# Kernel tuning notes

Measured on AMD Instinct MI355X. Metric: run time of the kernel, lower is better.

## Reference

```python
import jax, jax.numpy as jnp
import numpy as np

LAYER_SIZE = 8
STACK_SIZE = 2
RES_CH = 64
SKIP_CH = 128
N = 16
L = 8192
NUM_BLOCKS = LAYER_SIZE * STACK_SIZE


def _dilations():
    return [2 ** lev for _ in range(STACK_SIZE) for lev in range(LAYER_SIZE)]


def setup_inputs() -> dict:
    key = jax.random.key(0)
    k1, k2, k3, k4 = jax.random.split(key, 4)
    x = jax.random.normal(k1, (N, RES_CH, L), dtype=jnp.float32)
    # conv weights scaled ~1/sqrt(fan_in) to keep gates in a sane range
    W_dil = jax.random.normal(k2, (NUM_BLOCKS, RES_CH, RES_CH, 2), dtype=jnp.float32) * 0.088
    W_res = jax.random.normal(k3, (NUM_BLOCKS, RES_CH, RES_CH), dtype=jnp.float32) * 0.125
    W_skip = jax.random.normal(k4, (NUM_BLOCKS, SKIP_CH, RES_CH), dtype=jnp.float32) * 0.125
    return {"x": x, "W_dil": W_dil, "W_res": W_res, "W_skip": W_skip}


def reference(x, W_dil, W_res, W_skip):
    dilations = _dilations()
    out = x
    skips = []
    for i, d in enumerate(dilations):
        wd = W_dil[i]    # (Cout, Cin, 2)
        wr = W_res[i]    # (C, C) 1x1
        ws = W_skip[i]   # (S, C) 1x1
        # dilated causal conv, kernel_size=2, no padding -> length L-d
        y = (jnp.einsum('oi,nil->nol', wd[:, :, 0], out[:, :, :-d])
             + jnp.einsum('oi,nil->nol', wd[:, :, 1], out[:, :, d:]))
        # gated activation: tanh and sigmoid of the SAME dilated output
        g = jnp.tanh(y) * jax.nn.sigmoid(y)
        # NOTE: source has `if self.pooling > 1` with self.pooling a bool,
        # so AvgPool1d is never applied; pool_out == g always.
        res = jnp.einsum('oi,nil->nol', wr, g) + out[:, :, -g.shape[2]:]
        skips.append(jnp.einsum('oi,nil->nol', ws, g))
        out = res
    osize = out.shape[2]
    skip_out = skips[0][:, :, -osize:]
    for s in skips[1:]:
        skip_out = skip_out + s[:, :, -osize:]
    return (out, skip_out)
```

## Files before the change

### kernel.cpp

```cpp
#include <hip/hip_runtime.h>
#include <hip/hip_cooperative_groups.h>

namespace cg = cooperative_groups;


#define NBATCH 16
#define C 64
#define SC 128
#define L0 8192
#define OSIZE 7682
#define TILE 64
#define ST 128
#define FT 256
#define FW 384
#define FSMEM (8*FW*8*2 + 8*FT*8*2)

typedef __bf16 bf16x8 __attribute__((ext_vector_type(8)));
typedef __bf16 bf16x4 __attribute__((ext_vector_type(4)));
typedef float  f32x4  __attribute__((ext_vector_type(4)));

__global__ __launch_bounds__(256) void pack_weights(
    const float* __restrict__ Wd, const float* __restrict__ Wr,
    const float* __restrict__ Ws,
    __bf16* __restrict__ Wdm, __bf16* __restrict__ Wrm, __bf16* __restrict__ Wsm)
{
    int idx = blockIdx.x * 256 + threadIdx.x;
    if (idx < 131072) {
        int kp = idx & 127, o = (idx >> 7) & 63, ly = idx >> 13;
        int k = kp & 63, tap = kp >> 6;
        Wdm[idx] = (__bf16)Wd[(((ly * 64 + o) * 64 + k) << 1) + tap];
    } else if (idx < 196608) {
        int j = idx - 131072;
        Wrm[j] = (__bf16)Wr[j];
    } else if (idx < 327680) {
        int j = idx - 196608;
        Wsm[j] = (__bf16)Ws[j];
    }
}

__global__ __launch_bounds__(256, 2) void wavenet_fused(
    const float* __restrict__ x,
    float* __restrict__ bufA, float* __restrict__ bufB,
    const __bf16* __restrict__ Wdm, const __bf16* __restrict__ Wrm,
    const __bf16* __restrict__ Wsm,
    float* __restrict__ out, float* __restrict__ skip)
{
    extern __shared__ char smem[];
    __bf16* sxp = (__bf16*)smem;
    __bf16* sgp = (__bf16*)(smem + 8 * FW * 8 * 2);

    cg::grid_group gg = cg::this_grid();

    const int blk = blockIdx.x;
    const int n   = blk >> 5;
    const int a   = (blk & 31) * FT;
    const int t    = threadIdx.x;
    const int lane = t & 63;
    const int wv   = t >> 6;
    const int q    = lane >> 4;
    const int nn   = lane & 15;

    f32x4 accS[2][16];
    #pragma unroll
    for (int mt = 0; mt < 2; ++mt)
        #pragma unroll
        for (int nt = 0; nt < 16; ++nt)
            accS[mt][nt] = (f32x4){0.f, 0.f, 0.f, 0.f};

    const float* src = x;

    for (int ly = 0; ly < 16; ++ly) {
        const int d = 1 << (ly & 7);
        const int W = FT + d;

        for (int kg = 0; kg < 8; ++kg) {
            for (int j = t; j < W; j += 256) {
                int s = a - d + j;
                if (s < 0) s = 0;
                const float* col = src + (size_t)(n * C + kg * 8) * L0 + s;
                bf16x8 bv;
                #pragma unroll
                for (int jj = 0; jj < 8; ++jj) bv[jj] = (__bf16)col[(size_t)jj * L0];
                *(bf16x8*)(sxp + ((size_t)kg * FW + j) * 8) = bv;
            }
        }
        __syncthreads();

        const __bf16* arow = Wdm + ((size_t)ly * 64 + (wv * 16 + nn)) * 128 + q * 8;
        bf16x8 aW0 = *(const bf16x8*)(arow);
        bf16x8 aW1 = *(const bf16x8*)(arow + 32);
        bf16x8 aW2 = *(const bf16x8*)(arow + 64);
        bf16x8 aW3 = *(const bf16x8*)(arow + 96);
        #pragma unroll 4
        for (int nt = 0; nt < 16; ++nt) {
            int p = nt * 16 + nn;
            f32x4 acc = {0.f, 0.f, 0.f, 0.f};
            acc = __builtin_amdgcn_mfma_f32_16x16x32_bf16(aW0,
                    *(const bf16x8*)(sxp + ((size_t)(q    ) * FW + p    ) * 8), acc, 0, 0, 0);
            acc = __builtin_amdgcn_mfma_f32_16x16x32_bf16(aW1,
                    *(const bf16x8*)(sxp + ((size_t)(4 + q) * FW + p    ) * 8), acc, 0, 0, 0);
            acc = __builtin_amdgcn_mfma_f32_16x16x32_bf16(aW2,
                    *(const bf16x8*)(sxp + ((size_t)(q    ) * FW + p + d) * 8), acc, 0, 0, 0);
            acc = __builtin_amdgcn_mfma_f32_16x16x32_bf16(aW3,
                    *(const bf16x8*)(sxp + ((size_t)(4 + q) * FW + p + d) * 8), acc, 0, 0, 0);
            bf16x4 gv;
            #pragma unroll
            for (int r = 0; r < 4; ++r) {
                float y = fminf(fmaxf(acc[r], -20.f), 20.f);
                float u = __expf(y);
                gv[r] = (__bf16)(u * (u - 1.f) / fmaf(u, u, 1.f));
            }
            *(bf16x4*)(sgp + ((size_t)(2 * wv + (q >> 1)) * FT + p) * 8 + (q & 1) * 4) = gv;
        }
        __syncthreads();

        const __bf16* rrow = Wrm + ((size_t)ly * 64 + (wv * 16 + nn)) * 64 + q * 8;
        bf16x8 aR0 = *(const bf16x8*)rrow;
        bf16x8 aR1 = *(const bf16x8*)(rrow + 32);
        float* dst = (ly & 1) ? bufB : bufA;
        #pragma unroll 4
        for (int nt = 0; nt < 16; ++nt) {
            int p = nt * 16 + nn;
            f32x4 acc = {0.f, 0.f, 0.f, 0.f};
            acc = __builtin_amdgcn_mfma_f32_16x16x32_bf16(aR0,
                    *(const bf16x8*)(sgp + ((size_t)(q    ) * FT + p) * 8), acc, 0, 0, 0);
            acc = __builtin_amdgcn_mfma_f32_16x16x32_bf16(aR1,
                    *(const bf16x8*)(sgp + ((size_t)(4 + q) * FT + p) * 8), acc, 0, 0, 0);
            int s = a + p;
            if (ly == 15) {
                if (s >= 510) {
                    #pragma unroll
                    for (int r = 0; r < 4; ++r) {
                        int ch = wv * 16 + q * 4 + r;
                        out[(size_t)(n * C + ch) * OSIZE + (s - 510)]
                            = acc[r] + src[(size_t)(n * C + ch) * L0 + s];
                    }
                }
            } else {
                #pragma unroll
                for (int r = 0; r < 4; ++r) {
                    int ch = wv * 16 + q * 4 + r;
                    dst[(size_t)(n * C + ch) * L0 + s]
                        = acc[r] + src[(size_t)(n * C + ch) * L0 + s];
                }
            }
        }

        const __bf16* srow = Wsm + (size_t)ly * SC * 64;
        bf16x8 aS00 = *(const bf16x8*)(srow + (size_t)(wv * 32 +      nn) * 64 +      q * 8);
        bf16x8 aS01 = *(const bf16x8*)(srow + (size_t)(wv * 32 +      nn) * 64 + 32 + q * 8);
        bf16x8 aS10 = *(const bf16x8*)(srow + (size_t)(wv * 32 + 16 + nn) * 64 +      q * 8);
        bf16x8 aS11 = *(const bf16x8*)(srow + (size_t)(wv * 32 + 16 + nn) * 64 + 32 + q * 8);
        #pragma unroll
        for (int nt = 0; nt < 16; ++nt) {
            int p = nt * 16 + nn;
            bf16x8 b0 = *(const bf16x8*)(sgp + ((size_t)(q    ) * FT + p) * 8);
            bf16x8 b1 = *(const bf16x8*)(sgp + ((size_t)(4 + q) * FT + p) * 8);
            accS[0][nt] = __builtin_amdgcn_mfma_f32_16x16x32_bf16(aS00, b0, accS[0][nt], 0, 0, 0);
            accS[0][nt] = __builtin_amdgcn_mfma_f32_16x16x32_bf16(aS01, b1, accS[0][nt], 0, 0, 0);
            accS[1][nt] = __builtin_amdgcn_mfma_f32_16x16x32_bf16(aS10, b0, accS[1][nt], 0, 0, 0);
            accS[1][nt] = __builtin_amdgcn_mfma_f32_16x16x32_bf16(aS11, b1, accS[1][nt], 0, 0, 0);
        }

        src = dst;
        if (ly < 15) gg.sync();
    }

    #pragma unroll
    for (int mt = 0; mt < 2; ++mt)
        #pragma unroll
        for (int nt = 0; nt < 16; ++nt) {
            int s = a + nt * 16 + nn;
            if (s >= 510) {
                #pragma unroll
                for (int r = 0; r < 4; ++r) {
                    int sch = wv * 32 + mt * 16 + q * 4 + r;
                    skip[(size_t)(n * SC + sch) * OSIZE + (s - 510)] = accS[mt][nt][r];
                }
            }
        }
}

__global__ __launch_bounds__(256) void wavenet_layer_mfma(
    const float* __restrict__ src, int src_stride, int Lin,
    float* __restrict__ dst, int dst_stride,
    const __bf16* __restrict__ Wdm,
    const __bf16* __restrict__ Wrm,
    __bf16* __restrict__ gout,
    int d)
{
    extern __shared__ char smem_raw[];
    const int W    = TILE + d;
    const int Lout = Lin - d;
    const int n  = blockIdx.y;
    const int l0 = blockIdx.x * TILE;
    if (l0 >= Lout) return;
    const int np = min(TILE, Lout - l0);

    __bf16* sxp  = (__bf16*)smem_raw;
    float*  sres = (float*)(smem_raw + (size_t)8 * W * 8 * 2);
    __bf16* sgp  = (__bf16*)(sres + 64 * 65);

    const int t    = threadIdx.x;
    const int lane = t & 63;
    const int wv   = t >> 6;
    const int q    = lane >> 4;
    const int nn   = lane & 15;

    for (int item = t; item < 8 * W; item += 256) {
        int kg = item / W;
        int p  = item % W;
        bool inb = (l0 + p) < Lin;
        const float* col = src + (size_t)(n * C + kg * 8) * src_stride + l0 + p;
        float v[8];
        #pragma unroll
        for (int j = 0; j < 8; ++j) v[j] = inb ? col[(size_t)j * src_stride] : 0.f;
        bf16x8 bv;
        #pragma unroll
        for (int j = 0; j < 8; ++j) bv[j] = (__bf16)v[j];
        *(bf16x8*)(sxp + ((size_t)kg * W + p) * 8) = bv;
        int pr = p - d;
        if (pr >= 0 && pr < TILE) {
            #pragma unroll
            for (int j = 0; j < 8; ++j) sres[(kg * 8 + j) * 65 + pr] = v[j];
        }
    }
    __syncthreads();

    const __bf16* arow = Wdm + (size_t)(wv * 16 + nn) * 128 + q * 8;
    bf16x8 aW[4];
    #pragma unroll
    for (int ks = 0; ks < 4; ++ks) aW[ks] = *(const bf16x8*)(arow + ks * 32);

    #pragma unroll
    for (int nt = 0; nt < 4; ++nt) {
        int p0 = nt * 16;
        f32x4 acc = {0.f, 0.f, 0.f, 0.f};
        acc = __builtin_amdgcn_mfma_f32_16x16x32_bf16(aW[0],
                *(const bf16x8*)(sxp + ((size_t)(q    ) * W + p0 + nn    ) * 8), acc, 0, 0, 0);
        acc = __builtin_amdgcn_mfma_f32_16x16x32_bf16(aW[1],
                *(const bf16x8*)(sxp + ((size_t)(4 + q) * W + p0 + nn    ) * 8), acc, 0, 0, 0);
        acc = __builtin_amdgcn_mfma_f32_16x16x32_bf16(aW[2],
                *(const bf16x8*)(sxp + ((size_t)(q    ) * W + p0 + nn + d) * 8), acc, 0, 0, 0);
        acc = __builtin_amdgcn_mfma_f32_16x16x32_bf16(aW[3],
                *(const bf16x8*)(sxp + ((size_t)(4 + q) * W + p0 + nn + d) * 8), acc, 0, 0, 0);
        bf16x4 gv;
        #pragma unroll
        for (int r = 0; r < 4; ++r) {
            float y = fminf(fmaxf(acc[r], -20.f), 20.f);
            float u = __expf(y);
            gv[r] = (__bf16)(u * (u - 1.f) / fmaf(u, u, 1.f));
        }
        *(bf16x4*)(sgp + ((size_t)(2 * wv + (q >> 1)) * 64 + p0 + nn) * 8 + (q & 1) * 4) = gv;
    }
    __syncthreads();

    const __bf16* rrow = Wrm + (size_t)(wv * 16 + nn) * 64 + q * 8;
    bf16x8 aR0 = *(const bf16x8*)rrow;
    bf16x8 aR1 = *(const bf16x8*)(rrow + 32);
    #pragma unroll
    for (int nt = 0; nt < 4; ++nt) {
        int p0 = nt * 16;
        f32x4 acc = {0.f, 0.f, 0.f, 0.f};
        acc = __builtin_amdgcn_mfma_f32_16x16x32_bf16(aR0,
                *(const bf16x8*)(sgp + ((size_t)(q    ) * 64 + p0 + nn) * 8), acc, 0, 0, 0);
        acc = __builtin_amdgcn_mfma_f32_16x16x32_bf16(aR1,
                *(const bf16x8*)(sgp + ((size_t)(4 + q) * 64 + p0 + nn) * 8), acc, 0, 0, 0);
        if (p0 + nn < np) {
            #pragma unroll
            for (int r = 0; r < 4; ++r) {
                int ch = wv * 16 + q * 4 + r;
                dst[(size_t)(n * C + ch) * dst_stride + l0 + p0 + nn]
                    = acc[r] + sres[ch * 65 + p0 + nn];
            }
        }
    }

    const int sbase = Lout - OSIZE;
    for (int item = t; item < 8 * TILE; item += 256) {
        int p  = item & 63;
        int kg = item >> 6;
        int l  = l0 + p;
        if (l >= sbase && l < Lout) {
            *(bf16x8*)(gout + (((size_t)n * 8 + kg) * OSIZE + (l - sbase)) * 8)
                = *(const bf16x8*)(sgp + ((size_t)kg * 64 + p) * 8);
        }
    }
}

__global__ __launch_bounds__(256) void skip_gemm(
    const __bf16* __restrict__ g,
    const __bf16* __restrict__ Wsm,
    float* __restrict__ skip,
    int G, int lybase, int init)
{
    __shared__ __bf16 Bb[8][ST][8];
    const int n  = blockIdx.y;
    const int l0 = blockIdx.x * ST;
    const int t  = threadIdx.x;
    const int lane = t & 63;
    const int wv   = __builtin_amdgcn_readfirstlane(t >> 6);
    const int q = lane >> 4, nn = lane & 15;

    f32x4 acc[2][8];
    #pragma unroll
    for (int mt = 0; mt < 2; ++mt)
        #pragma unroll
        for (int nt = 0; nt < 8; ++nt) acc[mt][nt] = (f32x4){0.f, 0.f, 0.f, 0.f};

    for (int gi = 0; gi < G; ++gi) {
        const __bf16* gl = g + ((size_t)gi * NBATCH + n) * (size_t)8 * OSIZE * 8;
        #pragma unroll
        for (int j = 0; j < 4; ++j) {
            int kg   = 2 * wv + (j >> 1);
            int half = j & 1;
            const __bf16* srcp = gl + ((size_t)kg * OSIZE + l0 + half * 64) * 8
                                    + (size_t)lane * 8;
            __builtin_amdgcn_global_load_lds(
                (const __attribute__((address_space(1))) void*)srcp,
                (__attribute__((address_space(3))) void*)&Bb[kg][half * 64][0],
                16, 0, 0);
        }
        const __bf16* Wl = Wsm + (size_t)(lybase + gi) * SC * 64;
        bf16x8 a00 = *(const bf16x8*)(Wl + (size_t)(wv * 32 +      nn) * 64 +  0 + q * 8);
        bf16x8 a01 = *(const bf16x8*)(Wl + (size_t)(wv * 32 +      nn) * 64 + 32 + q * 8);
        bf16x8 a10 = *(const bf16x8*)(Wl + (size_t)(wv * 32 + 16 + nn) * 64 +  0 + q * 8);
        bf16x8 a11 = *(const bf16x8*)(Wl + (size_t)(wv * 32 + 16 + nn) * 64 + 32 + q * 8);
        __syncthreads();
        #pragma unroll
        for (int ks = 0; ks < 2; ++ks) {
            #pragma unroll
            for (int nt = 0; nt < 8; ++nt) {
                bf16x8 b = *(const bf16x8*)&Bb[ks * 4 + q][nt * 16 + nn][0];
                acc[0][nt] = __builtin_amdgcn_mfma_f32_16x16x32_bf16(
                                 ks ? a01 : a00, b, acc[0][nt], 0, 0, 0);
                acc[1][nt] = __builtin_amdgcn_mfma_f32_16x16x32_bf16(
                                 ks ? a11 : a10, b, acc[1][nt], 0, 0, 0);
            }
        }
        __syncthreads();
    }

    #pragma unroll
    for (int mt = 0; mt < 2; ++mt)
        #pragma unroll
        for (int nt = 0; nt < 8; ++nt) {
            int p = l0 + nt * 16 + nn;
            if (p < OSIZE) {
                #pragma unroll
                for (int r = 0; r < 4; ++r) {
                    int s = wv * 32 + mt * 16 + q * 4 + r;
                    size_t idx = ((size_t)n * SC + s) * OSIZE + p;
                    float v = acc[mt][nt][r];
                    skip[idx] = init ? v : (skip[idx] + v);
                }
            }
        }
}

extern "C" void kernel_launch(void* const* d_in, const int* in_sizes, int n_in,
                              void* d_out, int out_size, void* d_ws, size_t ws_size,
                              hipStream_t stream) {
    const float* x      = (const float*)d_in[0];
    const float* W_dil  = (const float*)d_in[1];
    const float* W_res  = (const float*)d_in[2];
    const float* W_skip = (const float*)d_in[3];

    float* out  = (float*)d_out;
    float* skip = out + (size_t)NBATCH * C * OSIZE;

    float*  bufA = (float*)d_ws;
    float*  bufB = bufA + (size_t)NBATCH * C * L0;
    __bf16* Wdm  = (__bf16*)(bufB + (size_t)NBATCH * C * L0);
    __bf16* Wrm  = Wdm + 16 * 64 * 128;
    __bf16* Wsm  = Wrm + 16 * 64 * 64;
    __bf16* gst  = Wsm + 16 * 128 * 64;

    static int use_coop = -1;
    if (use_coop < 0) {
        int dev = 0, coop = 0, nb = 0;
        hipGetDevice(&dev);
        hipDeviceGetAttribute(&coop, hipDeviceAttributeCooperativeLaunch, dev);
        hipError_t e = hipOccupancyMaxActiveBlocksPerMultiprocessor(
            &nb, (const void*)wavenet_fused, 256, FSMEM);
        use_coop = (coop && e == hipSuccess && nb >= 2) ? 1 : 0;
    }

    pack_weights<<<1280, 256, 0, stream>>>(W_dil, W_res, W_skip, Wdm, Wrm, Wsm);

    if (use_coop) {
        void* args[] = { (void*)&x, (void*)&bufA, (void*)&bufB,
                         (void*)&Wdm, (void*)&Wrm, (void*)&Wsm,
                         (void*)&out, (void*)&skip };
        hipLaunchCooperativeKernel((const void*)wavenet_fused,
                                   dim3(NBATCH * (L0 / FT)), dim3(256),
                                   args, FSMEM, stream);
        return;
    }

    const size_t slotHW = (size_t)NBATCH * 8 * OSIZE * 8;
    const size_t used   = (size_t)((char*)gst - (char*)d_ws);
    int G = 16;
    while (G > 1 && used + (size_t)G * slotHW * 2 + 65536 > ws_size) G >>= 1;

    const float* src = x;
    int src_stride = L0, Lin = L0;
    float* bufs[2] = {bufA, bufB};

    for (int i = 0; i < 16; ++i) {
        int d    = 1 << (i & 7);
        int Lout = Lin - d;
        float* dst;
        int dst_stride;
        if (i == 15) { dst = out;         dst_stride = OSIZE; }
        else         { dst = bufs[i & 1]; dst_stride = L0;    }

        int W = TILE + d;
        size_t smem = (size_t)128 * W + 64 * 65 * 4 + 8 * 64 * 8 * 2;

        dim3 grid((Lout + TILE - 1) / TILE, NBATCH);
        wavenet_layer_mfma<<<grid, 256, smem, stream>>>(
            src, src_stride, Lin, dst, dst_stride,
            Wdm + (size_t)i * 64 * 128,
            Wrm + (size_t)i * 64 * 64,
            gst + (size_t)(i % G) * slotHW,
            d);

        if (((i + 1) % G) == 0) {
            dim3 sgrid((OSIZE + ST - 1) / ST, NBATCH);
            skip_gemm<<<sgrid, 256, 0, stream>>>(
                gst, Wsm, skip, G, i + 1 - G, (i + 1 == G) ? 1 : 0);
        }

        src = dst;
        src_stride = dst_stride;
        Lin = Lout;
    }
}
```

Measured before the change: 601.3 us.

## Keep residual in registers and batch small-dilation layers with halo recompute

Each block now holds its residual tile in fp32 registers across layers instead of round-tripping through global buffers every layer. Layers with dilation 1–16 are run back-to-back on a 32-column halo staged once, recomputing the halo residuals locally in shared memory. This removes most grid-wide syncs and global writes and reads. Grid syncs and boundary writes to global memory remain only for the large-dilation layers. The cost is extra halo compute, more register pressure (xs plus accS), and larger shared memory use.

```diff
diff --git a/kernel.cpp b/kernel.cpp
--- a/kernel.cpp
+++ b/kernel.cpp
@@ -12,8 +12,7 @@
 #define TILE 64
 #define ST 128
 #define FT 256
-#define FW 384
-#define FSMEM (8*FW*8*2 + 8*FT*8*2)
+#define FSMEM 81920
 
 typedef __bf16 bf16x8 __attribute__((ext_vector_type(8)));
 typedef __bf16 bf16x4 __attribute__((ext_vector_type(4)));
@@ -40,69 +39,93 @@
 
 __global__ __launch_bounds__(256, 2) void wavenet_fused(
     const float* __restrict__ x,
-    float* __restrict__ bufA, float* __restrict__ bufB,
+    float* __restrict__ bufH0, float* __restrict__ bufH1,
     const __bf16* __restrict__ Wdm, const __bf16* __restrict__ Wrm,
     const __bf16* __restrict__ Wsm,
     float* __restrict__ out, float* __restrict__ skip)
 {
     extern __shared__ char smem[];
-    __bf16* sxp = (__bf16*)smem;
-    __bf16* sgp = (__bf16*)(smem + 8 * FW * 8 * 2);
-
     cg::grid_group gg = cg::this_grid();
 
-    const int blk = blockIdx.x;
-    const int n   = blk >> 5;
-    const int a   = (blk & 31) * FT;
+    const int blk  = blockIdx.x;
+    const int n    = blk >> 5;
+    const int a    = (blk & 31) * FT;
     const int t    = threadIdx.x;
     const int lane = t & 63;
     const int wv   = t >> 6;
     const int q    = lane >> 4;
     const int nn   = lane & 15;
-
+    const int kgw  = 2 * wv + (q >> 1);
+    const int hf4  = (q & 1) * 4;
+
+    f32x4 xs[16];
     f32x4 accS[2][16];
     #pragma unroll
     for (int mt = 0; mt < 2; ++mt)
         #pragma unroll
-        for (int nt = 0; nt < 16; ++nt)
-            accS[mt][nt] = (f32x4){0.f, 0.f, 0.f, 0.f};
-
-    const float* src = x;
-
-    for (int ly = 0; ly < 16; ++ly) {
-        const int d = 1 << (ly & 7);
-        const int W = FT + d;
-
-        for (int kg = 0; kg < 8; ++kg) {
-            for (int j = t; j < W; j += 256) {
-                int s = a - d + j;
-                if (s < 0) s = 0;
-                const float* col = src + (size_t)(n * C + kg * 8) * L0 + s;
-                bf16x8 bv;
+        for (int vt = 0; vt < 16; ++vt) accS[mt][vt] = (f32x4){0.f, 0.f, 0.f, 0.f};
+
+    #pragma unroll
+    for (int vt = 0; vt < 16; ++vt) {
+        const float* p = x + (size_t)(n * C + wv * 16 + q * 4) * L0 + a + vt * 16 + nn;
+        #pragma unroll
+        for (int r = 0; r < 4; ++r) xs[vt][r] = p[(size_t)r * L0];
+    }
+
+    __bf16* sxp = (__bf16*)smem;
+
+    auto stage_valid = [&](int SW, int SXO) {
+        #pragma unroll
+        for (int vt = 0; vt < 16; ++vt) {
+            bf16x4 v;
+            #pragma unroll
+            for (int r = 0; r < 4; ++r) v[r] = (__bf16)xs[vt][r];
+            *(bf16x4*)(sxp + (kgw * SW + SXO + vt * 16 + nn) * 8 + hf4) = v;
+        }
+    };
+    auto stage_halo = [&](int SW, int PH, const float* src, int H, int lg) {
+        for (int it = t; it < 8 * H; it += 256) {
+            int kg = it >> lg, hj = it & (H - 1);
+            int s = a - H + hj; if (s < 0) s = 0;
+            const float* col = src + (size_t)(n * C + kg * 8) * L0 + s;
+            bf16x8 bv;
+            #pragma unroll
+            for (int j = 0; j < 8; ++j) bv[j] = (__bf16)col[(size_t)j * L0];
+            *(bf16x8*)(sxp + (kg * SW + PH + hj) * 8) = bv;
+        }
+    };
+    auto bnd = [&](float* bufW, int VT0) {
+        #pragma unroll
+        for (int vt = 0; vt < 16; ++vt) {
+            if (vt >= VT0) {
+                float* p = bufW + (size_t)(n * C + wv * 16 + q * 4) * L0 + a + vt * 16 + nn;
                 #pragma unroll
-                for (int jj = 0; jj < 8; ++jj) bv[jj] = (__bf16)col[(size_t)jj * L0];
-                *(bf16x8*)(sxp + ((size_t)kg * FW + j) * 8) = bv;
-            }
-        }
-        __syncthreads();
-
-        const __bf16* arow = Wdm + ((size_t)ly * 64 + (wv * 16 + nn)) * 128 + q * 8;
+                for (int r = 0; r < 4; ++r) p[(size_t)r * L0] = xs[vt][r];
+            }
+        }
+        gg.sync();
+    };
+
+    auto do_layer = [&](int ly, int NT, int SW, int NTW, int CO,
+                        int ILp, int IRp, bool haloRes, bool writeSxp, bool isLast) {
+        __bf16* sgp = (__bf16*)(smem + SW * 128);
+        const __bf16* arow = Wdm + ((size_t)ly * 64 + wv * 16 + nn) * 128 + q * 8;
         bf16x8 aW0 = *(const bf16x8*)(arow);
         bf16x8 aW1 = *(const bf16x8*)(arow + 32);
         bf16x8 aW2 = *(const bf16x8*)(arow + 64);
         bf16x8 aW3 = *(const bf16x8*)(arow + 96);
-        #pragma unroll 4
-        for (int nt = 0; nt < 16; ++nt) {
-            int p = nt * 16 + nn;
+        #pragma unroll 2
+        for (int nt = 0; nt < NT; ++nt) {
+            int c = nt * 16 + nn;
             f32x4 acc = {0.f, 0.f, 0.f, 0.f};
             acc = __builtin_amdgcn_mfma_f32_16x16x32_bf16(aW0,
-                    *(const bf16x8*)(sxp + ((size_t)(q    ) * FW + p    ) * 8), acc, 0, 0, 0);
+                    *(const bf16x8*)(sxp + ((q    ) * SW + c + ILp) * 8), acc, 0, 0, 0);
             acc = __builtin_amdgcn_mfma_f32_16x16x32_bf16(aW1,
-                    *(const bf16x8*)(sxp + ((size_t)(4 + q) * FW + p    ) * 8), acc, 0, 0, 0);
+                    *(const bf16x8*)(sxp + ((4 + q) * SW + c + ILp) * 8), acc, 0, 0, 0);
             acc = __builtin_amdgcn_mfma_f32_16x16x32_bf16(aW2,
-                    *(const bf16x8*)(sxp + ((size_t)(q    ) * FW + p + d) * 8), acc, 0, 0, 0);
+                    *(const bf16x8*)(sxp + ((q    ) * SW + c + IRp) * 8), acc, 0, 0, 0);
             acc = __builtin_amdgcn_mfma_f32_16x16x32_bf16(aW3,
-                    *(const bf16x8*)(sxp + ((size_t)(4 + q) * FW + p + d) * 8), acc, 0, 0, 0);
+                    *(const bf16x8*)(sxp + ((4 + q) * SW + c + IRp) * 8), acc, 0, 0, 0);
             bf16x4 gv;
             #pragma unroll
             for (int r = 0; r < 4; ++r) {
@@ -110,72 +133,115 @@
                 float u = __expf(y);
                 gv[r] = (__bf16)(u * (u - 1.f) / fmaf(u, u, 1.f));
             }
-            *(bf16x4*)(sgp + ((size_t)(2 * wv + (q >> 1)) * FT + p) * 8 + (q & 1) * 4) = gv;
+            *(bf16x4*)(sgp + (kgw * NTW + c) * 8 + hf4) = gv;
         }
         __syncthreads();
 
-        const __bf16* rrow = Wrm + ((size_t)ly * 64 + (wv * 16 + nn)) * 64 + q * 8;
+        const __bf16* rrow = Wrm + ((size_t)ly * 64 + wv * 16 + nn) * 64 + q * 8;
         bf16x8 aR0 = *(const bf16x8*)rrow;
         bf16x8 aR1 = *(const bf16x8*)(rrow + 32);
-        float* dst = (ly & 1) ? bufB : bufA;
-        #pragma unroll 4
-        for (int nt = 0; nt < 16; ++nt) {
-            int p = nt * 16 + nn;
+        if (haloRes) {
+            #pragma unroll
+            for (int ht = 0; ht < 2; ++ht) {
+                int c = ht * 16 + nn;
+                f32x4 acc = {0.f, 0.f, 0.f, 0.f};
+                acc = __builtin_amdgcn_mfma_f32_16x16x32_bf16(aR0,
+                        *(const bf16x8*)(sgp + ((q    ) * NTW + c) * 8), acc, 0, 0, 0);
+                acc = __builtin_amdgcn_mfma_f32_16x16x32_bf16(aR1,
+                        *(const bf16x8*)(sgp + ((4 + q) * NTW + c) * 8), acc, 0, 0, 0);
+                __bf16* cell = sxp + (kgw * SW + 16 + c) * 8 + hf4;
+                bf16x4 xo = *(bf16x4*)cell, nw;
+                #pragma unroll
+                for (int r = 0; r < 4; ++r) nw[r] = (__bf16)(acc[r] + (float)xo[r]);
+                *(bf16x4*)cell = nw;
+            }
+        }
+        #pragma unroll
+        for (int vt = 0; vt < 16; ++vt) {
+            int c = CO + vt * 16 + nn;
             f32x4 acc = {0.f, 0.f, 0.f, 0.f};
             acc = __builtin_amdgcn_mfma_f32_16x16x32_bf16(aR0,
-                    *(const bf16x8*)(sgp + ((size_t)(q    ) * FT + p) * 8), acc, 0, 0, 0);
+                    *(const bf16x8*)(sgp + ((q    ) * NTW + c) * 8), acc, 0, 0, 0);
             acc = __builtin_amdgcn_mfma_f32_16x16x32_bf16(aR1,
-                    *(const bf16x8*)(sgp + ((size_t)(4 + q) * FT + p) * 8), acc, 0, 0, 0);
-            int s = a + p;
-            if (ly == 15) {
+                    *(const bf16x8*)(sgp + ((4 + q) * NTW + c) * 8), acc, 0, 0, 0);
+            #pragma unroll
+            for (int r = 0; r < 4; ++r) xs[vt][r] = acc[r] + xs[vt][r];
+            if (writeSxp) {
+                bf16x4 v;
+                #pragma unroll
+                for (int r = 0; r < 4; ++r) v[r] = (__bf16)xs[vt][r];
+                *(bf16x4*)(sxp + (kgw * SW + CO + 16 + vt * 16 + nn) * 8 + hf4) = v;
+            }
+            if (isLast) {
+                int s = a + vt * 16 + nn;
                 if (s >= 510) {
                     #pragma unroll
-                    for (int r = 0; r < 4; ++r) {
-                        int ch = wv * 16 + q * 4 + r;
-                        out[(size_t)(n * C + ch) * OSIZE + (s - 510)]
-                            = acc[r] + src[(size_t)(n * C + ch) * L0 + s];
-                    }
+                    for (int r = 0; r < 4; ++r)
+                        out[(size_t)(n * C + wv * 16 + q * 4 + r) * OSIZE + (s - 510)]
+                            = xs[vt][r];
                 }
-            } else {
-                #pragma unroll
-                for (int r = 0; r < 4; ++r) {
-                    int ch = wv * 16 + q * 4 + r;
-                    dst[(size_t)(n * C + ch) * L0 + s]
-                        = acc[r] + src[(size_t)(n * C + ch) * L0 + s];
-                }
             }
         }
 
         const __bf16* srow = Wsm + (size_t)ly * SC * 64;
-        bf16x8 aS00 = *(const bf16x8*)(srow + (size_t)(wv * 32 +      nn) * 64 +      q * 8);
-        bf16x8 aS01 = *(const bf16x8*)(srow + (size_t)(wv * 32 +      nn) * 64 + 32 + q * 8);
-        bf16x8 aS10 = *(const bf16x8*)(srow + (size_t)(wv * 32 + 16 + nn) * 64 +      q * 8);
-        bf16x8 aS11 = *(const bf16x8*)(srow + (size_t)(wv * 32 + 16 + nn) * 64 + 32 + q * 8);
-        #pragma unroll
-        for (int nt = 0; nt < 16; ++nt) {
-            int p = nt * 16 + nn;
-            bf16x8 b0 = *(const bf16x8*)(sgp + ((size_t)(q    ) * FT + p) * 8);
-            bf16x8 b1 = *(const bf16x8*)(sgp + ((size_t)(4 + q) * FT + p) * 8);
-            accS[0][nt] = __builtin_amdgcn_mfma_f32_16x16x32_bf16(aS00, b0, accS[0][nt], 0, 0, 0);
-            accS[0][nt] = __builtin_amdgcn_mfma_f32_16x16x32_bf16(aS01, b1, accS[0][nt], 0, 0, 0);
-            accS[1][nt] = __builtin_amdgcn_mfma_f32_16x16x32_bf16(aS10, b0, accS[1][nt], 0, 0, 0);
-            accS[1][nt] = __builtin_amdgcn_mfma_f32_16x16x32_bf16(aS11, b1, accS[1][nt], 0, 0, 0);
-        }
-
-        src = dst;
-        if (ly < 15) gg.sync();
+        bf16x8 aS00 = *(const bf16x8*)(srow + (wv * 32 +      nn) * 64 +      q * 8);
+        bf16x8 aS01 = *(const bf16x8*)(srow + (wv * 32 +      nn) * 64 + 32 + q * 8);
+        bf16x8 aS10 = *(const bf16x8*)(srow + (wv * 32 + 16 + nn) * 64 +      q * 8);
+        bf16x8 aS11 = *(const bf16x8*)(srow + (wv * 32 + 16 + nn) * 64 + 32 + q * 8);
+        #pragma unroll
+        for (int vt = 0; vt < 16; ++vt) {
+            int c = CO + vt * 16 + nn;
+            bf16x8 b0 = *(const bf16x8*)(sgp + ((q    ) * NTW + c) * 8);
+            bf16x8 b1 = *(const bf16x8*)(sgp + ((4 + q) * NTW + c) * 8);
+            accS[0][vt] = __builtin_amdgcn_mfma_f32_16x16x32_bf16(aS00, b0, accS[0][vt], 0, 0, 0);
+            accS[0][vt] = __builtin_amdgcn_mfma_f32_16x16x32_bf16(aS01, b1, accS[0][vt], 0, 0, 0);
+            accS[1][vt] = __builtin_amdgcn_mfma_f32_16x16x32_bf16(aS10, b0, accS[1][vt], 0, 0, 0);
+            accS[1][vt] = __builtin_amdgcn_mfma_f32_16x16x32_bf16(aS11, b1, accS[1][vt], 0, 0, 0);
+        }
+        __syncthreads();
+    };
+
+    float* hb[2] = {bufH0, bufH1};
+    const float* hsrc = x;
+    int p = 0;
+
+    #pragma unroll 1
+    for (int e = 0; e < 2; ++e) {
+        stage_valid(304, 48);
+        stage_halo(304, 16, hsrc, 32, 5);
+        __syncthreads();
+        #pragma unroll 1
+        for (int i = 0; i < 5; ++i) {
+            int d = 1 << i;
+            do_layer(e * 8 + i, 18, 304, 288, 32, 16 - d, 16, i < 4, i < 4, false);
+        }
+        #pragma unroll 1
+        for (int k = 0; k < 3; ++k) {
+            int d = 32 << k;
+            bnd(hb[p], 16 - (d >> 4));
+            hsrc = hb[p]; p ^= 1;
+            stage_valid(256 + d, d);
+            stage_halo(256 + d, 0, hsrc, d, 5 + k);
+            __syncthreads();
+            do_layer(e * 8 + 5 + k, 16, 256 + d, 256, 0, 0, d, false, false,
+                     (e == 1) && (k == 2));
+        }
+        if (e == 0) {
+            bnd(hb[p], 14);
+            hsrc = hb[p]; p ^= 1;
+        }
     }
 
     #pragma unroll
     for (int mt = 0; mt < 2; ++mt)
         #pragma unroll
-        for (int nt = 0; nt < 16; ++nt) {
-            int s = a + nt * 16 + nn;
+        for (int vt = 0; vt < 16; ++vt) {
+            int s = a + vt * 16 + nn;
             if (s >= 510) {
                 #pragma unroll
                 for (int r = 0; r < 4; ++r) {
                     int sch = wv * 32 + mt * 16 + q * 4 + r;
-                    skip[(size_t)(n * SC + sch) * OSIZE + (s - 510)] = accS[mt][nt][r];
+                    skip[(size_t)(n * SC + sch) * OSIZE + (s - 510)] = accS[mt][vt][r];
                 }
             }
         }
```

After: 601.7 us. No clear change (+0.1%).
